# Optimization experiments

Measured on AMD Instinct MI355X. Metric: run time of the kernel, lower is better.

Reference implementation:

```python
import jax, jax.numpy as jnp
import numpy as np

B, T, DM, H, DH, HID, GH, NMEM, TOPK = 2, 256, 512, 8, 64, 128, 64, 32768, 32


def setup_inputs() -> dict:
    key = jax.random.key(0)
    ks = jax.random.split(key, 16)
    s = 0.02
    return {
        "x": jax.random.normal(ks[0], (B, T, DM), jnp.float32),
        "Wq": jax.random.normal(ks[1], (DM, H * DH), jnp.float32) * s,
        "Wk": jax.random.normal(ks[2], (DM, H * DH), jnp.float32) * s,
        "Wv": jax.random.normal(ks[3], (DM, H * DH), jnp.float32) * s,
        "Wo": jax.random.normal(ks[4], (H * DH, DM), jnp.float32) * s,
        "Wg1": jax.random.normal(ks[5], (DM, GH), jnp.float32) * s,
        "bg1": jnp.zeros((GH,), jnp.float32),
        "Wg2": jax.random.normal(ks[6], (GH, H), jnp.float32) * s,
        "bg2": jnp.zeros((H,), jnp.float32),
        "Ws1": jax.random.normal(ks[7], (2 * DH, HID), jnp.float32) * s,
        "bs1": jnp.zeros((HID,), jnp.float32),
        "Ws2": jax.random.normal(ks[8], (HID,), jnp.float32) * s,
        "bs2": jnp.zeros((), jnp.float32),
        "mem_keys": jax.random.normal(ks[9], (NMEM, DH), jnp.float32),
        "mem_values": jax.random.normal(ks[10], (NMEM, DH), jnp.float32),
        "mem_topk": TOPK,
    }


def reference(x, Wq, Wk, Wv, Wo, Wg1, bg1, Wg2, bg2, Ws1, bs1, Ws2, bs2,
              mem_keys, mem_values, mem_topk):
    b, t, dm = x.shape
    # q/k/v projections: [B,T,H*Dh] -> [B,H,T,Dh]
    def shape_proj(y):
        return y.reshape(b, t, H, DH).transpose(0, 2, 1, 3)
    q = shape_proj(x @ Wq)
    k = shape_proj(x @ Wk)
    v = shape_proj(x @ Wv)

    # per-head, per-token gates in [0,1]: sigmoid(Linear(GELU(Linear(x))))
    gates = jnp.clip(jax.nn.sigmoid(jax.nn.gelu(x @ Wg1 + bg1) @ Wg2 + bg2), 0.0, 1.0)  # [B,T,H]

    # memory retrieval: top-k over dot-product scores of head-averaged query
    q_for_mem = q.mean(axis=1)                                   # [B,T,Dh]
    sel = jnp.einsum('btd,nd->btn', q_for_mem, mem_keys)         # [B,T,N]
    _, idx = jax.lax.top_k(sel, mem_topk)                        # [B,T,K]
    K_mem = mem_keys[idx]                                        # [B,T,K,Dh]
    V_mem = mem_values[idx]                                      # [B,T,K,Dh]

    # parametric score MLP: f([q;k]) = Ws2 . relu(W1q q + W1k k + bs1) + bs2
    W1q, W1k = Ws1[:DH], Ws1[DH:]
    hq = jnp.einsum('bhtd,df->bhtf', q, W1q) + bs1               # [B,H,T,F]
    hk_ctx = jnp.einsum('bhsd,df->bhsf', k, W1k)                 # [B,H,Tk,F]
    s_ctx = jnp.einsum('bhtsf,f->bhts',
                       jax.nn.relu(hq[:, :, :, None, :] + hk_ctx[:, :, None, :, :]),
                       Ws2) + bs2                                # [B,H,T,Tk]
    hk_mem = jnp.einsum('btkd,df->btkf', K_mem, W1k)             # [B,T,K,F]
    s_mem = jnp.einsum('bhtkf,f->bhtk',
                       jax.nn.relu(hq[:, :, :, None, :] + hk_mem[:, None, :, :, :]),
                       Ws2) + bs2                                # [B,H,T,K]

    w = jax.nn.softmax(jnp.concatenate([s_ctx, s_mem], axis=-1), axis=-1)
    tk = k.shape[2]
    w_ctx, w_mem = w[..., :tk], w[..., tk:]
    out = jnp.einsum('bhts,bhsd->bhtd', w_ctx, v) \
        + jnp.einsum('bhtk,btkd->bhtd', w_mem, V_mem)            # [B,H,T,Dh]

    out = out * gates.transpose(0, 2, 1)[..., None]              # gate per head/token
    y = out.transpose(0, 2, 1, 3).reshape(b, t, H * DH) @ Wo     # [B,T,Dm]
    return y
```

## Files before the change

### kernel.cpp

```cpp
#include <hip/hip_runtime.h>
#include <math.h>

#define B_ 2
#define T_ 256
#define DM_ 512
#define H_ 8
#define DH_ 64
#define HID_ 128
#define GH_ 64
#define NMEM_ 32768
#define TOPK_ 32
#define BT_ (B_*T_)
#define HD_ (H_*DH_)
#define SELC_ 8192
#define NCHUNK_ (NMEM_/SELC_)
#define TT_ 8
#define EQCAP_ 512
#define NTILE_ 256
#define CCAP_ 2048

__global__ __launch_bounds__(256) void awm_qkvg_kernel(
    const float* __restrict__ x,
    const float* __restrict__ Wq, const float* __restrict__ Wk, const float* __restrict__ Wv,
    const float* __restrict__ Wg1, const float* __restrict__ bg1,
    const float* __restrict__ Wg2, const float* __restrict__ bg2,
    float* __restrict__ q, float* __restrict__ k, float* __restrict__ v,
    float* __restrict__ gates) {
    int z = blockIdx.z;
    if (z == 3 && blockIdx.x != 0) return;
    const float* W = (z == 0) ? Wq : (z == 1) ? Wk : (z == 2) ? Wv : Wg1;
    float* C = (z == 0) ? q : (z == 1) ? k : v;
    const int N = (z == 3) ? GH_ : HD_;
    __shared__ float As[32][34];
    __shared__ float Bs[32][68];
    int bm = blockIdx.y * 32, bn = blockIdx.x * 64;
    int tid = threadIdx.x;
    int tm = (tid >> 4) * 2, tn = (tid & 15) * 4;
    float acc[2][4] = {};
    for (int k0 = 0; k0 < DM_; k0 += 32) {
        {
            int m = tid >> 3, kk = (tid & 7) * 4;
            float4 a = *(const float4*)&x[(size_t)(bm + m) * DM_ + k0 + kk];
            As[kk+0][m] = a.x; As[kk+1][m] = a.y; As[kk+2][m] = a.z; As[kk+3][m] = a.w;
#pragma unroll
            for (int p = 0; p < 2; ++p) {
                int idx = tid * 4 + p * 1024;
                int kb = idx >> 6, n = idx & 63;
                *(float4*)&Bs[kb][n] = *(const float4*)&W[(size_t)(k0 + kb) * N + bn + n];
            }
        }
        __syncthreads();
#pragma unroll
        for (int kk = 0; kk < 32; ++kk) {
            float2 a2 = *(const float2*)&As[kk][tm];
            float4 b4 = *(const float4*)&Bs[kk][tn];
            acc[0][0] += a2.x * b4.x; acc[0][1] += a2.x * b4.y;
            acc[0][2] += a2.x * b4.z; acc[0][3] += a2.x * b4.w;
            acc[1][0] += a2.y * b4.x; acc[1][1] += a2.y * b4.y;
            acc[1][2] += a2.y * b4.z; acc[1][3] += a2.y * b4.w;
        }
        __syncthreads();
    }
    if (z < 3) {
#pragma unroll
        for (int xr = 0; xr < 2; ++xr) {
            float4 r; r.x = acc[xr][0]; r.y = acc[xr][1]; r.z = acc[xr][2]; r.w = acc[xr][3];
            *(float4*)&C[(size_t)(bm + tm + xr) * HD_ + bn + tn] = r;
        }
    } else {
#pragma unroll
        for (int xr = 0; xr < 2; ++xr)
#pragma unroll
            for (int y = 0; y < 4; ++y) {
                float vv = acc[xr][y] + bg1[tn + y];
                float u = 0.7978845608028654f * (vv + 0.044715f * vv * vv * vv);
                Bs[tm + xr][tn + y] = 0.5f * vv * (1.f + tanhf(u));
            }
        float* wg = &As[0][0];
        for (int i = tid; i < GH_ * H_; i += 256) wg[i] = Wg2[i];
        __syncthreads();
        int r = tid >> 3, hh = tid & 7;
        float acg = bg2[hh];
#pragma unroll
        for (int j = 0; j < GH_; ++j) acg += Bs[r][j] * wg[j * H_ + hh];
        gates[(size_t)(bm + r) * H_ + hh] = 1.f / (1.f + expf(-acg));
    }
}

__global__ __launch_bounds__(256) void awm_out_kernel(
    const float* __restrict__ A, const float* __restrict__ W, float* __restrict__ C) {
    __shared__ float As[32][34];
    __shared__ float Bs[32][68];
    int bm = blockIdx.y * 32, bn = blockIdx.x * 64;
    int tid = threadIdx.x;
    int tm = (tid >> 4) * 2, tn = (tid & 15) * 4;
    float acc[2][4] = {};
    for (int k0 = 0; k0 < HD_; k0 += 32) {
        {
            int m = tid >> 3, kk = (tid & 7) * 4;
            float4 a = *(const float4*)&A[(size_t)(bm + m) * HD_ + k0 + kk];
            As[kk+0][m] = a.x; As[kk+1][m] = a.y; As[kk+2][m] = a.z; As[kk+3][m] = a.w;
#pragma unroll
            for (int p = 0; p < 2; ++p) {
                int idx = tid * 4 + p * 1024;
                int kb = idx >> 6, n = idx & 63;
                *(float4*)&Bs[kb][n] = *(const float4*)&W[(size_t)(k0 + kb) * DM_ + bn + n];
            }
        }
        __syncthreads();
#pragma unroll
        for (int kk = 0; kk < 32; ++kk) {
            float2 a2 = *(const float2*)&As[kk][tm];
            float4 b4 = *(const float4*)&Bs[kk][tn];
            acc[0][0] += a2.x * b4.x; acc[0][1] += a2.x * b4.y;
            acc[0][2] += a2.x * b4.z; acc[0][3] += a2.x * b4.w;
            acc[1][0] += a2.y * b4.x; acc[1][1] += a2.y * b4.y;
            acc[1][2] += a2.y * b4.z; acc[1][3] += a2.y * b4.w;
        }
        __syncthreads();
    }
#pragma unroll
    for (int xr = 0; xr < 2; ++xr) {
        float4 r; r.x = acc[xr][0]; r.y = acc[xr][1]; r.z = acc[xr][2]; r.w = acc[xr][3];
        *(float4*)&C[(size_t)(bm + tm + xr) * DM_ + bn + tn] = r;
    }
}

__global__ void awm_qmean_kernel(const float* __restrict__ q_flat, float* __restrict__ qm) {
    int i = blockIdx.x * 256 + threadIdx.x;
    if (i >= BT_ * DH_) return;
    int r = i / DH_, d = i % DH_;
    float acc = 0.f;
#pragma unroll
    for (int h = 0; h < H_; ++h) acc += q_flat[r * HD_ + h * DH_ + d];
    qm[i] = acc * 0.125f;
}

__global__ __launch_bounds__(256) void awm_selgemm_kernel(
    const float* __restrict__ qm, const float* __restrict__ mkeys,
    float* __restrict__ selc, float* __restrict__ tmax, int chunk0, int ld) {
    __shared__ float Qs[32][68];
    __shared__ float Ks[32][132];
    int bn = blockIdx.x * 128;
    int bm = blockIdx.y * 64;
    int tid = threadIdx.x;
    int tm = (tid >> 4) * 4;
    int tn = (tid & 15) * 8;
    float acc[4][8] = {};
    for (int kc = 0; kc < 2; ++kc) {
        if (kc) __syncthreads();
#pragma unroll
        for (int p = 0; p < 2; ++p) {
            int i4 = tid * 4 + p * 1024;
            int m = i4 >> 5, d = i4 & 31;
            float4 a = *(const float4*)&qm[(size_t)(bm + m) * DH_ + kc * 32 + d];
            int s = (d >> 2) & 7;
            int mc = (((m >> 2) ^ s) << 2) + (m & 3);
            Qs[d+0][mc] = a.x; Qs[d+1][mc] = a.y; Qs[d+2][mc] = a.z; Qs[d+3][mc] = a.w;
        }
#pragma unroll
        for (int p = 0; p < 4; ++p) {
            int i4 = tid * 4 + p * 1024;
            int n = i4 >> 5, d = i4 & 31;
            float4 a = *(const float4*)&mkeys[(size_t)(chunk0 + bn + n) * DH_ + kc * 32 + d];
            int s = (d >> 2) & 7;
            int nc = (((n >> 2) ^ s) << 2) + (n & 3);
            Ks[d+0][nc] = a.x; Ks[d+1][nc] = a.y; Ks[d+2][nc] = a.z; Ks[d+3][nc] = a.w;
        }
        __syncthreads();
#pragma unroll 8
        for (int d = 0; d < 32; ++d) {
            int s = (d >> 2) & 7;
            int tmw = ((tm >> 2) ^ s) << 2;
            int b0i = ((tn >> 2) ^ s) << 2;
            int b1i = (((tn >> 2) + 1) ^ s) << 2;
            float4 a4 = *(const float4*)&Qs[d][tmw];
            float4 b0 = *(const float4*)&Ks[d][b0i];
            float4 b1 = *(const float4*)&Ks[d][b1i];
            float av[4] = {a4.x, a4.y, a4.z, a4.w};
            float bv[8] = {b0.x, b0.y, b0.z, b0.w, b1.x, b1.y, b1.z, b1.w};
#pragma unroll
            for (int x = 0; x < 4; ++x)
#pragma unroll
                for (int y = 0; y < 8; ++y) acc[x][y] += av[x] * bv[y];
        }
    }
#pragma unroll
    for (int x = 0; x < 4; ++x) {
        float* cp = &selc[(size_t)(bm + tm + x) * ld + bn + tn];
        float4 r0, r1;
        r0.x = acc[x][0]; r0.y = acc[x][1]; r0.z = acc[x][2]; r0.w = acc[x][3];
        r1.x = acc[x][4]; r1.y = acc[x][5]; r1.z = acc[x][6]; r1.w = acc[x][7];
        *(float4*)cp = r0; *(float4*)(cp + 4) = r1;
    }
    {
        int tile = (chunk0 + bn) >> 7;
#pragma unroll
        for (int x = 0; x < 4; ++x) {
            float m = acc[x][0];
#pragma unroll
            for (int y = 1; y < 8; ++y) m = fmaxf(m, acc[x][y]);
#pragma unroll
            for (int o = 1; o < 16; o <<= 1) m = fmaxf(m, __shfl_xor(m, o));
            if ((tid & 15) == 0) tmax[(size_t)(bm + tm + x) * NTILE_ + tile] = m;
        }
    }
}

__device__ __forceinline__ float awm_sort64_f32(float x, int l) {
#pragma unroll
    for (int k = 2; k <= 64; k <<= 1) {
#pragma unroll
        for (int j = k >> 1; j > 0; j >>= 1) {
            float y = __shfl_xor(x, j);
            bool takeMax = (((l & k) == 0) == ((l & j) == 0));
            float mx = fmaxf(x, y), mn = fminf(x, y);
            x = takeMax ? mx : mn;
        }
    }
    return x;
}
__device__ __forceinline__ unsigned long long awm_sort64_u64(unsigned long long x, int l) {
#pragma unroll
    for (int k = 2; k <= 64; k <<= 1) {
#pragma unroll
        for (int j = k >> 1; j > 0; j >>= 1) {
            unsigned long long y = __shfl_xor(x, j);
            bool takeMax = (((l & k) == 0) == ((l & j) == 0));
            unsigned long long mx = x > y ? x : y;
            unsigned long long mn = x > y ? y : x;
            x = takeMax ? mx : mn;
        }
    }
    return x;
}
__device__ __forceinline__ unsigned long long awm_merge64_u64(unsigned long long x, int l) {
#pragma unroll
    for (int j = 32; j > 0; j >>= 1) {
        unsigned long long y = __shfl_xor(x, j);
        bool takeMax = ((l & j) == 0);
        unsigned long long mx = x > y ? x : y;
        unsigned long long mn = x > y ? y : x;
        x = takeMax ? mx : mn;
    }
    return x;
}

__device__ __forceinline__ unsigned awm_ordkey(float f) {
    unsigned u = __float_as_uint(f);
    return u ^ ((unsigned)((int)u >> 31) | 0x80000000u);
}

__global__ __launch_bounds__(256) void awm_selfilter_kernel(
    const float* __restrict__ selc, const float* __restrict__ tmax,
    int* __restrict__ topidx) {
    int r = blockIdx.x;
    int tid = threadIdx.x;
    int w = tid >> 6, l = tid & 63;
    __shared__ int tlist[NTILE_];
    __shared__ int ctrs[2];
    __shared__ unsigned long long cand[CCAP_];
    __shared__ unsigned long long wtop[128];
    if (tid < 2) ctrs[tid] = 0;
    float4 m4 = *(const float4*)&tmax[(size_t)r * NTILE_ + (l << 2)];
    float lm = fmaxf(fmaxf(m4.x, m4.y), fmaxf(m4.z, m4.w));
    float sx = awm_sort64_f32(lm, l);
    float s = __shfl(sx, 31);
    __syncthreads();
    {
        float mt = tmax[(size_t)r * NTILE_ + tid];
        if (mt >= s) { int p = atomicAdd(&ctrs[0], 1); tlist[p] = tid; }
    }
    __syncthreads();
    int nt = ctrs[0];
    for (int i = tid; i < nt * 32; i += 256) {
        int tile = tlist[i >> 5];
        int col = (tile << 7) + ((i & 31) << 2);
        float4 v4 = *(const float4*)&selc[(size_t)r * NMEM_ + col];
        float fv[4] = {v4.x, v4.y, v4.z, v4.w};
#pragma unroll
        for (int c2 = 0; c2 < 4; ++c2) {
            if (fv[c2] >= s) {
                int p = atomicAdd(&ctrs[1], 1);
                if (p < CCAP_)
                    cand[p] = ((unsigned long long)awm_ordkey(fv[c2]) << 32)
                            | (unsigned long long)(0xFFFFFFFFu - (unsigned)(col + c2));
            }
        }
    }
    __syncthreads();
    int ne = ctrs[1]; if (ne > CCAP_) ne = CCAP_;
    int nch = (ne + 63) >> 6;
    unsigned long long run = 0ull;
    for (int c = w; c < nch; c += 4) {
        int j = (c << 6) + l;
        unsigned long long xx = (j < ne) ? cand[j] : 0ull;
        xx = awm_sort64_u64(xx, l);
        unsigned long long rv = __shfl(xx, 63 - l);
        run = (run > rv) ? run : rv;
        run = awm_merge64_u64(run, l);
    }
    if (l < 32) wtop[w * 32 + l] = run;
    __syncthreads();
    if (w == 0) {
        unsigned long long a = (l < 32) ? wtop[l] : wtop[32 + (63 - l)];
        a = awm_merge64_u64(a, l);
        unsigned long long b = (l < 32) ? wtop[64 + l] : wtop[96 + (63 - l)];
        b = awm_merge64_u64(b, l);
        unsigned long long z = (l < 32) ? a : __shfl(b, 63 - l);
        z = awm_merge64_u64(z, l);
        if (l < 32)
            topidx[r * TOPK_ + l] =
                (int)(0xFFFFFFFFu - (unsigned)(z & 0xFFFFFFFFull));
    }
}

__global__ __launch_bounds__(256) void awm_seltop_kernel(
    const float* __restrict__ selc, int ld, int chunk_arg,
    float* __restrict__ cand_val, int* __restrict__ cand_idx) {
    int r = blockIdx.x;
    int chunk = (chunk_arg >= 0) ? chunk_arg : (int)blockIdx.y;
    int col0 = (ld == NMEM_) ? chunk * SELC_ : 0;
    int tid = threadIdx.x;
    __shared__ unsigned hist[4096];
    __shared__ float eqv[EQCAP_];
    __shared__ unsigned eqi[EQCAP_];
    __shared__ float abv_v[32];
    __shared__ unsigned abv_i[32];
    __shared__ int ctrs[2];
    __shared__ int binfo[1];
    for (int i = tid; i < 4096; i += 256) hist[i] = 0u;
    if (tid < 2) ctrs[tid] = 0;
    if (tid == 0) binfo[0] = 0;
    __syncthreads();
    const float* src = selc + (size_t)r * ld + col0;
    float4 vv[8];
#pragma unroll
    for (int p = 0; p < 8; ++p)
        vv[p] = *(const float4*)&src[(tid << 2) + (p << 10)];
#pragma unroll
    for (int p = 0; p < 8; ++p) {
        atomicAdd(&hist[awm_ordkey(vv[p].x) >> 20], 1u);
        atomicAdd(&hist[awm_ordkey(vv[p].y) >> 20], 1u);
        atomicAdd(&hist[awm_ordkey(vv[p].z) >> 20], 1u);
        atomicAdd(&hist[awm_ordkey(vv[p].w) >> 20], 1u);
    }
    __syncthreads();
    if (tid < 64) {
        int lane = tid;
        unsigned s = 0;
        for (int j = 0; j < 64; ++j)
            s += hist[(lane << 6) + ((j + lane) & 63)];
        unsigned suf = s;
#pragma unroll
        for (int off = 1; off < 64; off <<= 1) {
            unsigned t2 = __shfl_down(suf, off);
            suf += (lane + off < 64) ? t2 : 0u;
        }
        unsigned nd = __shfl_down(suf, 1);
        unsigned nxt = (lane == 63) ? 0u : nd;
        bool cross = (suf >= (unsigned)TOPK_) && (nxt < (unsigned)TOPK_);
        unsigned long long mc = __ballot(cross ? 1 : 0);
        int sstar = (mc == 0ull) ? 63 : (int)__builtin_ctzll(mc);
        unsigned above_super = (mc == 0ull) ? 0u : __shfl(nxt, sstar);
        unsigned suf2 = hist[(sstar << 6) + lane];
#pragma unroll
        for (int off = 1; off < 64; off <<= 1) {
            unsigned t2 = __shfl_down(suf2, off);
            suf2 += (lane + off < 64) ? t2 : 0u;
        }
        unsigned tot = suf2 + above_super;
        unsigned nd2 = __shfl_down(tot, 1);
        unsigned nxt2 = (lane == 63) ? above_super : nd2;
        bool cross2 = (tot >= (unsigned)TOPK_) && (nxt2 < (unsigned)TOPK_);
        if (cross2) binfo[0] = (sstar << 6) + lane;
    }
    __syncthreads();
    int theta = binfo[0];
    int gbase = chunk * SELC_;
#pragma unroll
    for (int p = 0; p < 8; ++p) {
        float fv[4] = {vv[p].x, vv[p].y, vv[p].z, vv[p].w};
#pragma unroll
        for (int c = 0; c < 4; ++c) {
            int bin = (int)(awm_ordkey(fv[c]) >> 20);
            if (bin >= theta) {
                unsigned li = (unsigned)((tid << 2) + (p << 10) + c);
                if (bin > theta) {
                    int pos = atomicAdd(&ctrs[0], 1);
                    if (pos < 32) { abv_v[pos] = fv[c]; abv_i[pos] = li; }
                } else {
                    int pos = atomicAdd(&ctrs[1], 1);
                    if (pos < EQCAP_) { eqv[pos] = fv[c]; eqi[pos] = li; }
                }
            }
        }
    }
    __syncthreads();
    if (tid < 64) {
        int lane = tid;
        int na = ctrs[0]; if (na > TOPK_) na = TOPK_;
        int ne = ctrs[1]; if (ne > EQCAP_) ne = EQCAP_;
        float* cvp = cand_val + (size_t)r * 128 + chunk * 32;
        int* cip = cand_idx + (size_t)r * 128 + chunk * 32;
        if (lane < na) { cvp[lane] = abv_v[lane]; cip[lane] = gbase + (int)abv_i[lane]; }
        int need = TOPK_ - na;
        unsigned deadm = 0u;
        for (int it = 0; it < need; ++it) {
            float bv = -INFINITY; unsigned bi = 0xFFFFFFFFu; int bs = -1;
            int jj = 0;
            for (int j = lane; j < ne; j += 64, ++jj) {
                if (!((deadm >> jj) & 1u)) {
                    float vq = eqv[j]; unsigned iq = eqi[j];
                    if (vq > bv || (vq == bv && iq < bi)) { bv = vq; bi = iq; bs = j; }
                }
            }
#pragma unroll
            for (int off = 32; off > 0; off >>= 1) {
                float ov = __shfl_xor(bv, off);
                unsigned oi = __shfl_xor(bi, off);
                int os = __shfl_xor(bs, off);
                if (ov > bv || (ov == bv && oi < bi)) { bv = ov; bi = oi; bs = os; }
            }
            if (lane == 0) {
                int gi = (bi == 0xFFFFFFFFu) ? gbase : (gbase + (int)bi);
                cvp[na + it] = bv; cip[na + it] = gi;
            }
            if (bs >= 0 && (bs & 63) == lane) deadm |= (1u << (bs >> 6));
        }
    }
}

__global__ __launch_bounds__(64) void awm_merge_kernel(
    const float* __restrict__ cand_val, const int* __restrict__ cand_idx,
    int* __restrict__ topidx) {
    int r = blockIdx.x;
    int lane = threadIdx.x;
    float v0 = cand_val[(size_t)r * 128 + lane];
    float v1 = cand_val[(size_t)r * 128 + 64 + lane];
    int i0 = cand_idx[(size_t)r * 128 + lane];
    int i1 = cand_idx[(size_t)r * 128 + 64 + lane];
    for (int it = 0; it < TOPK_; ++it) {
        float v; int ix;
        if (v0 > v1 || (v0 == v1 && i0 < i1)) { v = v0; ix = i0; } else { v = v1; ix = i1; }
#pragma unroll
        for (int off = 32; off > 0; off >>= 1) {
            float ov = __shfl_xor(v, off);
            int oi = __shfl_xor(ix, off);
            if (ov > v || (ov == v && oi < ix)) { v = ov; ix = oi; }
        }
        if (lane == 0) topidx[r * TOPK_ + it] = ix;
        if (ix == i0) v0 = -INFINITY;
        else if (ix == i1) v1 = -INFINITY;
    }
}

__global__ __launch_bounds__(256) void awm_hid_kernel(
    const float* __restrict__ q_flat, const float* __restrict__ k_flat,
    const float* __restrict__ Ws1, const float* __restrict__ bs1,
    float* __restrict__ hq, float* __restrict__ hkc) {
    int isK = blockIdx.y;
    int bm = blockIdx.x * 32;
    int tid = threadIdx.x;
    __shared__ float As[64][34];
    __shared__ float Ws_s[64][132];
    const float* src = isK ? k_flat : q_flat;
    const float* W = Ws1 + (isK ? (size_t)DH_ * HID_ : 0);
    {
        int m = tid >> 3, kq = (tid & 7) * 8;
        int rho = bm + m;
        int bh = rho >> 8, t = rho & 255;
        int b = bh >> 3, h = bh & 7;
        const float* sp = src + (size_t)(b * T_ + t) * HD_ + h * DH_ + kq;
        float4 a = *(const float4*)sp;
        float4 c = *(const float4*)(sp + 4);
        As[kq+0][m] = a.x; As[kq+1][m] = a.y; As[kq+2][m] = a.z; As[kq+3][m] = a.w;
        As[kq+4][m] = c.x; As[kq+5][m] = c.y; As[kq+6][m] = c.z; As[kq+7][m] = c.w;
    }
    for (int i = tid; i < 64 * HID_ / 4; i += 256) {
        int k = (i * 4) >> 7, f = (i * 4) & 127;
        *(float4*)&Ws_s[k][f] = *(const float4*)&W[(size_t)k * HID_ + f];
    }
    __syncthreads();
    int tm = (tid >> 4) * 2, tn = (tid & 15) * 8;
    float acc[2][8] = {};
#pragma unroll 8
    for (int k = 0; k < DH_; ++k) {
        float2 a2 = *(const float2*)&As[k][tm];
        float4 b0 = *(const float4*)&Ws_s[k][tn];
        float4 b1 = *(const float4*)&Ws_s[k][tn + 4];
        float av[2] = {a2.x, a2.y};
        float bv[8] = {b0.x, b0.y, b0.z, b0.w, b1.x, b1.y, b1.z, b1.w};
#pragma unroll
        for (int x = 0; x < 2; ++x)
#pragma unroll
            for (int y = 0; y < 8; ++y) acc[x][y] += av[x] * bv[y];
    }
    float* out = isK ? hkc : hq;
#pragma unroll
    for (int x = 0; x < 2; ++x) {
        int rho = bm + tm + x;
        float vv[8];
#pragma unroll
        for (int y = 0; y < 8; ++y)
            vv[y] = acc[x][y] + (isK ? 0.f : bs1[tn + y]);
        float4 r0, r1;
        r0.x = vv[0]; r0.y = vv[1]; r0.z = vv[2]; r0.w = vv[3];
        r1.x = vv[4]; r1.y = vv[5]; r1.z = vv[6]; r1.w = vv[7];
        float* op = out + (size_t)rho * HID_ + tn;
        *(float4*)op = r0; *(float4*)(op + 4) = r1;
    }
}

__global__ __launch_bounds__(256) void awm_smem_kernel(
    const float* __restrict__ hq, const float* __restrict__ mkeys,
    const int* __restrict__ topidx, const float* __restrict__ Ws1,
    const float* __restrict__ Ws2, float* __restrict__ smem_out) {
    int bt = blockIdx.x;
    int b = bt >> 8, t = bt & 255;
    int tid = threadIdx.x;
    __shared__ float W1k_s[32][132];
    __shared__ float mk_s[64][36];
    __shared__ float hkm_s[32][133];
    __shared__ float hq_s[8][132];
    __shared__ float w2_s[HID_];
    __shared__ int key_s[TOPK_];
    {
        int h = tid >> 5, fq = (tid & 31) * 4;
        *(float4*)&hq_s[h][fq] =
            *(const float4*)&hq[((size_t)(b * H_ + h) * T_ + t) * HID_ + fq];
    }
    if (tid < HID_) w2_s[tid] = Ws2[tid];
    if (tid < TOPK_) key_s[tid] = topidx[bt * TOPK_ + tid];
    __syncthreads();
    {
        int j = tid >> 3, kq = (tid & 7) * 8;
        const float* sp = mkeys + (size_t)key_s[j] * DH_ + kq;
        float4 a = *(const float4*)sp;
        float4 c = *(const float4*)(sp + 4);
        mk_s[kq+0][j] = a.x; mk_s[kq+1][j] = a.y; mk_s[kq+2][j] = a.z; mk_s[kq+3][j] = a.w;
        mk_s[kq+4][j] = c.x; mk_s[kq+5][j] = c.y; mk_s[kq+6][j] = c.z; mk_s[kq+7][j] = c.w;
    }
    int j0 = (tid >> 5) * 4, f0 = (tid & 31) * 4;
    float acc[4][4] = {};
    for (int kc = 0; kc < 2; ++kc) {
        __syncthreads();
        for (int i = tid; i < 32 * HID_ / 4; i += 256) {
            int k = (i * 4) >> 7, f = (i * 4) & 127;
            *(float4*)&W1k_s[k][f] =
                *(const float4*)&Ws1[(size_t)(DH_ + kc * 32 + k) * HID_ + f];
        }
        __syncthreads();
#pragma unroll 8
        for (int k = 0; k < 32; ++k) {
            float4 a4 = *(const float4*)&mk_s[kc * 32 + k][j0];
            float4 b4 = *(const float4*)&W1k_s[k][f0];
            float av[4] = {a4.x, a4.y, a4.z, a4.w};
            float bv[4] = {b4.x, b4.y, b4.z, b4.w};
#pragma unroll
            for (int x = 0; x < 4; ++x)
#pragma unroll
                for (int y = 0; y < 4; ++y) acc[x][y] += av[x] * bv[y];
        }
    }
#pragma unroll
    for (int x = 0; x < 4; ++x)
#pragma unroll
        for (int y = 0; y < 4; ++y) hkm_s[j0 + x][f0 + y] = acc[x][y];
    __syncthreads();
    int h = tid >> 5, j = tid & 31;
    float sacc = 0.f;
#pragma unroll 8
    for (int f = 0; f < HID_; ++f) {
        float u = hq_s[h][f] + hkm_s[j][f];
        sacc += fmaxf(u, 0.f) * w2_s[f];
    }
    smem_out[((size_t)(b * H_ + h) * T_ + t) * TOPK_ + j] = sacc;
}

__global__ __launch_bounds__(256) void awm_attn2_kernel(
    const float* __restrict__ hq, const float* __restrict__ hkc,
    const float* __restrict__ smem_in, const float* __restrict__ v_flat,
    const float* __restrict__ mem_values, const int* __restrict__ topidx,
    const float* __restrict__ Ws2, const float* __restrict__ gates,
    float* __restrict__ outg) {
    int tb = blockIdx.x;
    int bh = blockIdx.y;
    int b = bh >> 3, h = bh & 7;
    int tbase = tb * TT_;
    int tid = threadIdx.x;
    __shared__ float hq_s[HID_][TT_ + 2];
    __shared__ float hk_s[32][260];
    __shared__ float sc[TT_][292];
    __shared__ float w2_s[HID_];
    __shared__ int idx_s[TT_][TOPK_];
    {
        int t = tid >> 5, fq = (tid & 31) * 4;
        float4 a = *(const float4*)&hq[((size_t)bh * T_ + tbase + t) * HID_ + fq];
        hq_s[fq+0][t] = a.x; hq_s[fq+1][t] = a.y; hq_s[fq+2][t] = a.z; hq_s[fq+3][t] = a.w;
    }
    if (tid < HID_) w2_s[tid] = Ws2[tid];
    {
        int t = tid >> 5, j = tid & 31;
        sc[t][256 + j] = smem_in[((size_t)bh * T_ + tbase + t) * TOPK_ + j];
        idx_s[t][j] = topidx[((size_t)b * T_ + tbase + t) * TOPK_ + j];
    }
    int t0 = (tid >> 6) * 2, s0 = (tid & 63) * 4;
    float acc[2][4] = {};
    for (int fc = 0; fc < 4; ++fc) {
        __syncthreads();
        {
            int f4 = (tid & 7) * 4, sr = tid >> 3;
#pragma unroll
            for (int p = 0; p < 8; ++p) {
                int s = sr + p * 32;
                float4 a = *(const float4*)&hkc[((size_t)bh * T_ + s) * HID_ + fc * 32 + f4];
                hk_s[f4+0][s] = a.x; hk_s[f4+1][s] = a.y; hk_s[f4+2][s] = a.z; hk_s[f4+3][s] = a.w;
            }
        }
        __syncthreads();
#pragma unroll 8
        for (int f = 0; f < 32; ++f) {
            float2 a2 = *(const float2*)&hq_s[fc * 32 + f][t0];
            float4 b4 = *(const float4*)&hk_s[f][s0];
            float w2f = w2_s[fc * 32 + f];
            float av[2] = {a2.x, a2.y};
            float bv[4] = {b4.x, b4.y, b4.z, b4.w};
#pragma unroll
            for (int x = 0; x < 2; ++x)
#pragma unroll
                for (int y = 0; y < 4; ++y)
                    acc[x][y] += fmaxf(av[x] + bv[y], 0.f) * w2f;
        }
    }
    {
        float4 r0, r1;
        r0.x = acc[0][0]; r0.y = acc[0][1]; r0.z = acc[0][2]; r0.w = acc[0][3];
        r1.x = acc[1][0]; r1.y = acc[1][1]; r1.z = acc[1][2]; r1.w = acc[1][3];
        *(float4*)&sc[t0][s0] = r0;
        *(float4*)&sc[t0 + 1][s0] = r1;
    }
    __syncthreads();
    {
        int t = tid >> 5, l = tid & 31;
        float mx = -INFINITY;
#pragma unroll
        for (int k = 0; k < 9; ++k) mx = fmaxf(mx, sc[t][l + 32 * k]);
#pragma unroll
        for (int off = 16; off > 0; off >>= 1) mx = fmaxf(mx, __shfl_xor(mx, off, 32));
        float sum = 0.f;
#pragma unroll
        for (int k = 0; k < 9; ++k) {
            float e = expf(sc[t][l + 32 * k] - mx);
            sc[t][l + 32 * k] = e;
            sum += e;
        }
#pragma unroll
        for (int off = 16; off > 0; off >>= 1) sum += __shfl_xor(sum, off, 32);
        float inv = 1.f / sum;
#pragma unroll
        for (int k = 0; k < 9; ++k) sc[t][l + 32 * k] *= inv;
    }
    __syncthreads();
    {
        int g = tid >> 6, l = tid & 63;
        int ta = 2 * g, tbb = 2 * g + 1;
        const float* vb = v_flat + (size_t)b * T_ * HD_ + h * DH_ + l;
        float a0 = 0.f, a1 = 0.f;
#pragma unroll 8
        for (int s = 0; s < T_; ++s) {
            float vv = vb[(size_t)s * HD_];
            a0 += sc[ta][s] * vv;
            a1 += sc[tbb][s] * vv;
        }
#pragma unroll 4
        for (int j = 0; j < TOPK_; ++j) {
            a0 += sc[ta][256 + j] * mem_values[(size_t)idx_s[ta][j] * DH_ + l];
            a1 += sc[tbb][256 + j] * mem_values[(size_t)idx_s[tbb][j] * DH_ + l];
        }
        float g0 = gates[(size_t)(b * T_ + tbase + ta) * H_ + h];
        float g1v = gates[(size_t)(b * T_ + tbase + tbb) * H_ + h];
        outg[(size_t)(b * T_ + tbase + ta) * HD_ + h * DH_ + l] = a0 * g0;
        outg[(size_t)(b * T_ + tbase + tbb) * HD_ + h * DH_ + l] = a1 * g1v;
    }
}

extern "C" void kernel_launch(void* const* d_in, const int* in_sizes, int n_in,
                              void* d_out, int out_size, void* d_ws, size_t ws_size,
                              hipStream_t stream) {
    (void)in_sizes; (void)n_in; (void)out_size;
    const float* x    = (const float*)d_in[0];
    const float* Wq   = (const float*)d_in[1];
    const float* Wk   = (const float*)d_in[2];
    const float* Wv   = (const float*)d_in[3];
    const float* Wo   = (const float*)d_in[4];
    const float* Wg1  = (const float*)d_in[5];
    const float* bg1  = (const float*)d_in[6];
    const float* Wg2  = (const float*)d_in[7];
    const float* bg2  = (const float*)d_in[8];
    const float* Ws1  = (const float*)d_in[9];
    const float* bs1  = (const float*)d_in[10];
    const float* Ws2  = (const float*)d_in[11];
    const float* mk   = (const float*)d_in[13];
    const float* mv   = (const float*)d_in[14];
    float* y = (float*)d_out;

    float* w = (float*)d_ws;
    size_t off = 0;
    float* q_flat = w + off; off += (size_t)BT_ * HD_;
    float* k_flat = w + off; off += (size_t)BT_ * HD_;
    float* v_flat = w + off; off += (size_t)BT_ * HD_;
    float* gates  = w + off; off += (size_t)BT_ * H_;
    float* qm     = w + off; off += (size_t)BT_ * DH_;
    float* hq     = w + off; off += (size_t)B_ * H_ * T_ * HID_;
    float* hkc    = w + off; off += (size_t)B_ * H_ * T_ * HID_;
    float* smemb  = w + off; off += (size_t)B_ * H_ * T_ * TOPK_;
    float* outg   = w + off; off += (size_t)BT_ * HD_;
    float* cand_v = w + off; off += (size_t)BT_ * 128;
    int*   cand_i = (int*)(w + off); off += (size_t)BT_ * 128;
    int*   topidx = (int*)(w + off); off += (size_t)BT_ * TOPK_;
    float* tmax   = w + off; off += (size_t)BT_ * NTILE_;
    float* selc   = w + off;
    int fullw = (ws_size >= (off + (size_t)BT_ * NMEM_) * sizeof(float));

    dim3 thr256(256);
    awm_qkvg_kernel<<<dim3(8, 16, 4), thr256, 0, stream>>>(
        x, Wq, Wk, Wv, Wg1, bg1, Wg2, bg2, q_flat, k_flat, v_flat, gates);
    awm_qmean_kernel<<<dim3((BT_ * DH_ + 255) / 256), thr256, 0, stream>>>(q_flat, qm);
    if (fullw) {
        awm_selgemm_kernel<<<dim3(NMEM_ / 128, BT_ / 64), thr256, 0, stream>>>(
            qm, mk, selc, tmax, 0, NMEM_);
        awm_selfilter_kernel<<<dim3(BT_), thr256, 0, stream>>>(selc, tmax, topidx);
    } else {
        for (int c = 0; c < NCHUNK_; ++c) {
            awm_selgemm_kernel<<<dim3(SELC_ / 128, BT_ / 64), thr256, 0, stream>>>(
                qm, mk, selc, tmax, c * SELC_, SELC_);
            awm_seltop_kernel<<<dim3(BT_, 1), thr256, 0, stream>>>(
                selc, SELC_, c, cand_v, cand_i);
        }
        awm_merge_kernel<<<dim3(BT_), dim3(64), 0, stream>>>(cand_v, cand_i, topidx);
    }
    awm_hid_kernel<<<dim3(B_ * H_ * T_ / 32, 2), thr256, 0, stream>>>(
        q_flat, k_flat, Ws1, bs1, hq, hkc);
    awm_smem_kernel<<<dim3(BT_), thr256, 0, stream>>>(hq, mk, topidx, Ws1, Ws2, smemb);
    awm_attn2_kernel<<<dim3(T_ / TT_, B_ * H_), thr256, 0, stream>>>(
        hq, hkc, smemb, v_flat, mv, topidx, Ws2, gates, outg);
    awm_out_kernel<<<dim3(8, 16), thr256, 0, stream>>>(outg, Wo, y);
}
```

Measured before the change: 144.9 us.

## Fuse head-mean into selection GEMM and widen attention tile to 16 tokens

The separate q-mean kernel is removed. Each selection-GEMM block now computes the head-averaged query rows itself from q_flat and writes them directly into its shared-memory tile, which saves one launch and a global round trip. The attention kernel now handles 16 tokens per block with 512 threads, halving the grid and reusing each loaded hk tile across more tokens. The risks are redundant mean computation across the column blocks of the selection GEMM and lower occupancy from the larger shared-memory footprint per block.

```diff
diff --git a/kernel.cpp b/kernel.cpp
--- a/kernel.cpp
+++ b/kernel.cpp
@@ -14,7 +14,7 @@
 #define HD_ (H_*DH_)
 #define SELC_ 8192
 #define NCHUNK_ (NMEM_/SELC_)
-#define TT_ 8
+#define TT_ 16
 #define EQCAP_ 512
 #define NTILE_ 256
 #define CCAP_ 2048
@@ -126,18 +126,8 @@
     }
 }
 
-__global__ void awm_qmean_kernel(const float* __restrict__ q_flat, float* __restrict__ qm) {
-    int i = blockIdx.x * 256 + threadIdx.x;
-    if (i >= BT_ * DH_) return;
-    int r = i / DH_, d = i % DH_;
-    float acc = 0.f;
-#pragma unroll
-    for (int h = 0; h < H_; ++h) acc += q_flat[r * HD_ + h * DH_ + d];
-    qm[i] = acc * 0.125f;
-}
-
 __global__ __launch_bounds__(256) void awm_selgemm_kernel(
-    const float* __restrict__ qm, const float* __restrict__ mkeys,
+    const float* __restrict__ q_flat, const float* __restrict__ mkeys,
     float* __restrict__ selc, float* __restrict__ tmax, int chunk0, int ld) {
     __shared__ float Qs[32][68];
     __shared__ float Ks[32][132];
@@ -146,17 +136,34 @@
     int tid = threadIdx.x;
     int tm = (tid >> 4) * 4;
     int tn = (tid & 15) * 8;
+    int m_ = tid >> 2, dq = (tid & 3) * 16;
+    float4 qmr[4];
+    {
+        const float* qp = q_flat + (size_t)(bm + m_) * HD_ + dq;
+#pragma unroll
+        for (int qq = 0; qq < 4; ++qq) {
+            float4 s0 = {0.f, 0.f, 0.f, 0.f};
+#pragma unroll
+            for (int h = 0; h < 8; ++h) {
+                float4 a = *(const float4*)&qp[h * DH_ + qq * 4];
+                s0.x += a.x; s0.y += a.y; s0.z += a.z; s0.w += a.w;
+            }
+            qmr[qq].x = s0.x * 0.125f; qmr[qq].y = s0.y * 0.125f;
+            qmr[qq].z = s0.z * 0.125f; qmr[qq].w = s0.w * 0.125f;
+        }
+    }
     float acc[4][8] = {};
     for (int kc = 0; kc < 2; ++kc) {
         if (kc) __syncthreads();
-#pragma unroll
-        for (int p = 0; p < 2; ++p) {
-            int i4 = tid * 4 + p * 1024;
-            int m = i4 >> 5, d = i4 & 31;
-            float4 a = *(const float4*)&qm[(size_t)(bm + m) * DH_ + kc * 32 + d];
-            int s = (d >> 2) & 7;
-            int mc = (((m >> 2) ^ s) << 2) + (m & 3);
-            Qs[d+0][mc] = a.x; Qs[d+1][mc] = a.y; Qs[d+2][mc] = a.z; Qs[d+3][mc] = a.w;
+        if ((dq >> 5) == kc) {
+#pragma unroll
+            for (int qq = 0; qq < 4; ++qq) {
+                int dl = dq - kc * 32 + qq * 4;
+                int s = (dl >> 2) & 7;
+                int mc = (((m_ >> 2) ^ s) << 2) + (m_ & 3);
+                Qs[dl+0][mc] = qmr[qq].x; Qs[dl+1][mc] = qmr[qq].y;
+                Qs[dl+2][mc] = qmr[qq].z; Qs[dl+3][mc] = qmr[qq].w;
+            }
         }
 #pragma unroll
         for (int p = 0; p < 4; ++p) {
@@ -578,7 +585,7 @@
     smem_out[((size_t)(b * H_ + h) * T_ + t) * TOPK_ + j] = sacc;
 }
 
-__global__ __launch_bounds__(256) void awm_attn2_kernel(
+__global__ __launch_bounds__(512) void awm_attn2_kernel(
     const float* __restrict__ hq, const float* __restrict__ hkc,
     const float* __restrict__ smem_in, const float* __restrict__ v_flat,
     const float* __restrict__ mem_values, const int* __restrict__ topidx,
@@ -612,8 +619,8 @@
         {
             int f4 = (tid & 7) * 4, sr = tid >> 3;
 #pragma unroll
-            for (int p = 0; p < 8; ++p) {
-                int s = sr + p * 32;
+            for (int p = 0; p < 4; ++p) {
+                int s = sr + p * 64;
                 float4 a = *(const float4*)&hkc[((size_t)bh * T_ + s) * HID_ + fc * 32 + f4];
                 hk_s[f4+0][s] = a.x; hk_s[f4+1][s] = a.y; hk_s[f4+2][s] = a.z; hk_s[f4+3][s] = a.w;
             }
@@ -711,7 +718,6 @@
     float* k_flat = w + off; off += (size_t)BT_ * HD_;
     float* v_flat = w + off; off += (size_t)BT_ * HD_;
     float* gates  = w + off; off += (size_t)BT_ * H_;
-    float* qm     = w + off; off += (size_t)BT_ * DH_;
     float* hq     = w + off; off += (size_t)B_ * H_ * T_ * HID_;
     float* hkc    = w + off; off += (size_t)B_ * H_ * T_ * HID_;
     float* smemb  = w + off; off += (size_t)B_ * H_ * T_ * TOPK_;
@@ -726,15 +732,14 @@
     dim3 thr256(256);
     awm_qkvg_kernel<<<dim3(8, 16, 4), thr256, 0, stream>>>(
         x, Wq, Wk, Wv, Wg1, bg1, Wg2, bg2, q_flat, k_flat, v_flat, gates);
-    awm_qmean_kernel<<<dim3((BT_ * DH_ + 255) / 256), thr256, 0, stream>>>(q_flat, qm);
     if (fullw) {
         awm_selgemm_kernel<<<dim3(NMEM_ / 128, BT_ / 64), thr256, 0, stream>>>(
-            qm, mk, selc, tmax, 0, NMEM_);
+            q_flat, mk, selc, tmax, 0, NMEM_);
         awm_selfilter_kernel<<<dim3(BT_), thr256, 0, stream>>>(selc, tmax, topidx);
     } else {
         for (int c = 0; c < NCHUNK_; ++c) {
             awm_selgemm_kernel<<<dim3(SELC_ / 128, BT_ / 64), thr256, 0, stream>>>(
-                qm, mk, selc, tmax, c * SELC_, SELC_);
+                q_flat, mk, selc, tmax, c * SELC_, SELC_);
             awm_seltop_kernel<<<dim3(BT_, 1), thr256, 0, stream>>>(
                 selc, SELC_, c, cand_v, cand_i);
         }
@@ -743,7 +748,7 @@
     awm_hid_kernel<<<dim3(B_ * H_ * T_ / 32, 2), thr256, 0, stream>>>(
         q_flat, k_flat, Ws1, bs1, hq, hkc);
     awm_smem_kernel<<<dim3(BT_), thr256, 0, stream>>>(hq, mk, topidx, Ws1, Ws2, smemb);
-    awm_attn2_kernel<<<dim3(T_ / TT_, B_ * H_), thr256, 0, stream>>>(
+    awm_attn2_kernel<<<dim3(T_ / TT_, B_ * H_), dim3(512), 0, stream>>>(
         hq, hkc, smemb, v_flat, mv, topidx, Ws2, gates, outg);
     awm_out_kernel<<<dim3(8, 16), thr256, 0, stream>>>(outg, Wo, y);
 }
```

Result: slower. 151.9 us (+4.8%).
